# Kernel optimization log

Hardware: AMD Instinct MI355X
Metric: run time of the kernel (lower is better)

The kernel has to match this reference:

```python
import jax, jax.numpy as jnp
import numpy as np

W_MATCH, W_POS, W_COV = 1.0, 1.0, 0.1  # SetLoss init kwargs (w_rot unused in 3dpos path)


def setup_inputs() -> dict:
    key = jax.random.key(0)
    ks = jax.random.split(key, 6)
    bs, n, m = 4096, 31, 31
    B = bs * (n + 1)          # bs*(n+1) groups
    N = B * n                 # flattened rows
    # scores are 'in log space negative' -> use -softplus(randn)
    scores = -jax.nn.softplus(jax.random.normal(ks[0], (B, n + 1, m + 1), jnp.float32))
    indices = jax.random.randint(ks[1], (B, n, 1), -1, m)           # -1 = no prediction
    cov = jax.random.uniform(ks[2], (B, n, 1), jnp.float32, 0.1, 1.1)  # positive variances
    pos = jax.random.normal(ks[3], (B, n, 3), jnp.float32)
    pose = jax.random.normal(ks[4], (N, 7), jnp.float32)
    match = jax.random.randint(ks[5], (N, 1), -1, m)                # -1 = no label
    return {"scores": scores, "cov": cov, "pos": pos, "pose": pose,
            "indices": indices, "match": match}


def _masked_mean(vals, msk, default):
    cnt = msk.sum()
    s = jnp.where(msk, vals, 0.0).sum()
    return jnp.where(cnt > 0, s / jnp.maximum(cnt, 1).astype(vals.dtype), default)


def reference(scores, cov, pos, pose, indices, match):
    # SetLoss.forward(out, target, 'match_3dpos')
    m = scores.shape[2] - 1
    # ---- loss_match_func ----
    label_valid = match[:, 0] != -1                       # [N]
    li = jnp.where(match == -1, m, match)                 # route -1 to dustbin column m
    sc = scores[:, :-1, :].reshape(-1, m + 1)             # [N, m+1]
    cost = -jnp.take_along_axis(sc, li, axis=1)           # [N, 1]
    loss_match = cost.mean()
    oi = indices.reshape(-1, 1)
    success = (oi == match)[:, 0].astype(jnp.float32)     # [N]
    pred_valid = oi[:, 0] != -1
    recall = _masked_mean(success, label_valid, jnp.float32(1.0))
    precision = _masked_mean(success, pred_valid, jnp.float32(1.0))
    # ---- position MSE ----
    pos_f = pos.reshape(-1, 3)                            # [N, 3]
    d = pos_f - pose[:, :3]
    loss_pos = jnp.mean(d * d) * 3.0
    loss_rot = jnp.float32(0.0)
    # ---- diagonal-covariance NLL (loss_cov_func, dim=3, cov col repeated x3) ----
    # diag cov [c,c,c]: inverse = 1/c per entry, det = c**3
    c = cov.reshape(-1)                                   # [N]
    weighted = jnp.sum(d * d, axis=-1) / c                # diff^T Sigma^{-1} diff
    per = weighted + 3.0 * jnp.log(c) * 0.04              # + 0.04 * log det
    loss_cov = _masked_mean(per, pred_valid, jnp.float32(5.0))
    total = W_MATCH * loss_match + W_POS * loss_pos + W_COV * loss_cov
    return total, loss_match, loss_pos, loss_rot, loss_cov, precision, recall
```

## Files before the change

### kernel.cpp

```cpp
#include <hip/hip_runtime.h>
#include <hip/hip_bf16.h>

#define NRED 7

__device__ __forceinline__ float waveReduce(float v) {
#pragma unroll
    for (int o = 32; o > 0; o >>= 1) v += __shfl_down(v, o, 64);
    return v;
}

__global__ void setloss_partial(const float* __restrict__ scores,
                                const float* __restrict__ cov,
                                const float* __restrict__ pos,
                                const float* __restrict__ pose,
                                const int* __restrict__ indices,
                                const int* __restrict__ match,
                                float* __restrict__ part,
                                int N, int grid) {
    float acc[NRED];
#pragma unroll
    for (int k = 0; k < NRED; ++k) acc[k] = 0.0f;

    const int stride = gridDim.x * blockDim.x;
    for (int r = blockIdx.x * blockDim.x + threadIdx.x; r < N; r += stride) {
        const unsigned ur = (unsigned)r;
        const unsigned b  = ur / 31u;
        const unsigned i  = ur - b * 31u;

        const int mt = match[r];
        const int li = (mt < 0) ? 31 : mt;
        const float sc = scores[(size_t)(((b << 5) + i) << 5) + (unsigned)li];
        acc[0] -= sc;

        const int oi = indices[r];
        const float succ = (oi == mt) ? 1.0f : 0.0f;
        const bool lv = (mt != -1);
        const bool pv = (oi != -1);
        acc[1] += lv ? 1.0f : 0.0f;
        acc[2] += lv ? succ : 0.0f;
        acc[3] += pv ? 1.0f : 0.0f;
        acc[4] += pv ? succ : 0.0f;

        const float px = pos[3 * (size_t)r + 0];
        const float py = pos[3 * (size_t)r + 1];
        const float pz = pos[3 * (size_t)r + 2];
        const float qx = pose[7 * (size_t)r + 0];
        const float qy = pose[7 * (size_t)r + 1];
        const float qz = pose[7 * (size_t)r + 2];
        const float dx = px - qx, dy = py - qy, dz = pz - qz;
        const float d2 = dx * dx + dy * dy + dz * dz;
        acc[5] += d2;

        const float c = cov[r];
        if (pv) acc[6] += d2 / c + 0.12f * logf(c);
    }

    __shared__ float sdata[NRED][4];
    const int lane = threadIdx.x & 63;
    const int wave = threadIdx.x >> 6;
#pragma unroll
    for (int k = 0; k < NRED; ++k) {
        float v = waveReduce(acc[k]);
        if (lane == 0) sdata[k][wave] = v;
    }
    __syncthreads();
    if (threadIdx.x == 0) {
#pragma unroll
        for (int k = 0; k < NRED; ++k) {
            float v = sdata[k][0] + sdata[k][1] + sdata[k][2] + sdata[k][3];
            part[(size_t)k * grid + blockIdx.x] = v;
        }
    }
}

__global__ void setloss_final(const float* __restrict__ part, int grid,
                              float* __restrict__ out, int N) {
    float acc[NRED];
#pragma unroll
    for (int k = 0; k < NRED; ++k) acc[k] = 0.0f;
    for (int t = threadIdx.x; t < grid; t += blockDim.x) {
#pragma unroll
        for (int k = 0; k < NRED; ++k) acc[k] += part[(size_t)k * grid + t];
    }
    __shared__ float sdata[NRED][4];
    const int lane = threadIdx.x & 63;
    const int wave = threadIdx.x >> 6;
#pragma unroll
    for (int k = 0; k < NRED; ++k) {
        float v = waveReduce(acc[k]);
        if (lane == 0) sdata[k][wave] = v;
    }
    __syncthreads();
    if (threadIdx.x == 0) {
        float s[NRED];
#pragma unroll
        for (int k = 0; k < NRED; ++k)
            s[k] = sdata[k][0] + sdata[k][1] + sdata[k][2] + sdata[k][3];

        const float fN = (float)N;
        const float loss_match = s[0] / fN;
        const float loss_pos   = s[5] / fN;
        const float cnt_label  = s[1];
        const float cnt_pred   = s[3];
        const float recall     = (cnt_label > 0.0f) ? s[2] / cnt_label : 1.0f;
        const float precision  = (cnt_pred  > 0.0f) ? s[4] / cnt_pred  : 1.0f;
        const float loss_cov   = (cnt_pred  > 0.0f) ? s[6] / cnt_pred  : 5.0f;
        const float total = 1.0f * loss_match + 1.0f * loss_pos + 0.1f * loss_cov;

        out[0] = total;
        out[1] = loss_match;
        out[2] = loss_pos;
        out[3] = 0.0f;
        out[4] = loss_cov;
        out[5] = precision;
        out[6] = recall;
    }
}

extern "C" void kernel_launch(void* const* d_in, const int* in_sizes, int n_in,
                              void* d_out, int out_size, void* d_ws, size_t ws_size,
                              hipStream_t stream) {
    const float* scores  = (const float*)d_in[0];
    const float* cov     = (const float*)d_in[1];
    const float* pos     = (const float*)d_in[2];
    const float* pose    = (const float*)d_in[3];
    const int*   indices = (const int*)d_in[4];
    const int*   match   = (const int*)d_in[5];
    float* out = (float*)d_out;

    const int N = in_sizes[5];

    int grid = 2048;
    const size_t need = (size_t)NRED * (size_t)grid * sizeof(float);
    if (ws_size < need) grid = (int)(ws_size / ((size_t)NRED * sizeof(float)));
    if (grid < 1) grid = 1;

    float* part = (float*)d_ws;

    setloss_partial<<<grid, 256, 0, stream>>>(scores, cov, pos, pose, indices,
                                              match, part, N, grid);
    setloss_final<<<1, 256, 0, stream>>>(part, grid, out, N);
}
```

Baseline: 133.6 us.

## Vectorize row loads four-at-a-time and size grid to one chunk per thread

Each thread now processes four consecutive rows, loading match/indices/cov with int4/float4 and the pos and pose rows with several float4 loads, instead of strided scalar loads. The grid is sized so each thread handles about one chunk, giving far more blocks than the previous fixed 2048. This targets the poorly coalesced strided loads of the 3- and 7-wide rows. In exchange, the pose loads now pull all 7 columns, including the 4 unused ones, and the final reduction must sum many more partials.

```diff
diff --git a/kernel.cpp b/kernel.cpp
--- a/kernel.cpp
+++ b/kernel.cpp
@@ -9,50 +9,76 @@
     return v;
 }
 
-__global__ void setloss_partial(const float* __restrict__ scores,
-                                const float* __restrict__ cov,
-                                const float* __restrict__ pos,
-                                const float* __restrict__ pose,
-                                const int* __restrict__ indices,
-                                const int* __restrict__ match,
-                                float* __restrict__ part,
-                                int N, int grid) {
+__device__ __forceinline__ void rowAcc(int r, int mt, int oi, float c,
+                                       float px, float py, float pz,
+                                       float qx, float qy, float qz,
+                                       const float* __restrict__ scores,
+                                       float acc[NRED]) {
+    const unsigned ur = (unsigned)r;
+    const unsigned b  = ur / 31u;
+    const unsigned i  = ur - b * 31u;
+    const int li = (mt < 0) ? 31 : mt;
+    const float sc = scores[(size_t)b * 1024u + i * 32u + (unsigned)li];
+    acc[0] -= sc;
+
+    const float succ = (oi == mt) ? 1.0f : 0.0f;
+    const bool lv = (mt != -1);
+    const bool pv = (oi != -1);
+    acc[1] += lv ? 1.0f : 0.0f;
+    acc[2] += lv ? succ : 0.0f;
+    acc[3] += pv ? 1.0f : 0.0f;
+    acc[4] += pv ? succ : 0.0f;
+
+    const float dx = px - qx, dy = py - qy, dz = pz - qz;
+    const float d2 = dx * dx + dy * dy + dz * dz;
+    acc[5] += d2;
+    if (pv) acc[6] += d2 / c + 0.12f * logf(c);
+}
+
+__global__ __launch_bounds__(256) void setloss_partial(
+        const float* __restrict__ scores,
+        const float* __restrict__ cov,
+        const float* __restrict__ pos,
+        const float* __restrict__ pose,
+        const int* __restrict__ indices,
+        const int* __restrict__ match,
+        float* __restrict__ part,
+        int N, int grid, int nChunk) {
     float acc[NRED];
 #pragma unroll
     for (int k = 0; k < NRED; ++k) acc[k] = 0.0f;
 
-    const int stride = gridDim.x * blockDim.x;
-    for (int r = blockIdx.x * blockDim.x + threadIdx.x; r < N; r += stride) {
-        const unsigned ur = (unsigned)r;
-        const unsigned b  = ur / 31u;
-        const unsigned i  = ur - b * 31u;
+    const int tstride = grid * 256;
+    for (int chunk = blockIdx.x * 256 + threadIdx.x; chunk < nChunk; chunk += tstride) {
+        const int base = chunk * 4;
+        if (base + 3 < N) {
+            const int4   mm = *(const int4*)  (match   + base);
+            const int4   oo = *(const int4*)  (indices + base);
+            const float4 cc = *(const float4*)(cov     + base);
+            const float* pp = pos  + 3 * (size_t)base;
+            const float4 p0 = *(const float4*)(pp + 0);
+            const float4 p1 = *(const float4*)(pp + 4);
+            const float4 p2 = *(const float4*)(pp + 8);
+            const float* qq = pose + 7 * (size_t)base;
+            const float4 q0 = *(const float4*)(qq + 0);
+            const float4 q1 = *(const float4*)(qq + 4);
+            const float4 q2 = *(const float4*)(qq + 8);
+            const float4 q3 = *(const float4*)(qq + 12);
+            const float4 q4 = *(const float4*)(qq + 16);
+            const float4 q5 = *(const float4*)(qq + 20);
 
-        const int mt = match[r];
-        const int li = (mt < 0) ? 31 : mt;
-        const float sc = scores[(size_t)(((b << 5) + i) << 5) + (unsigned)li];
-        acc[0] -= sc;
-
-        const int oi = indices[r];
-        const float succ = (oi == mt) ? 1.0f : 0.0f;
-        const bool lv = (mt != -1);
-        const bool pv = (oi != -1);
-        acc[1] += lv ? 1.0f : 0.0f;
-        acc[2] += lv ? succ : 0.0f;
-        acc[3] += pv ? 1.0f : 0.0f;
-        acc[4] += pv ? succ : 0.0f;
-
-        const float px = pos[3 * (size_t)r + 0];
-        const float py = pos[3 * (size_t)r + 1];
-        const float pz = pos[3 * (size_t)r + 2];
-        const float qx = pose[7 * (size_t)r + 0];
-        const float qy = pose[7 * (size_t)r + 1];
-        const float qz = pose[7 * (size_t)r + 2];
-        const float dx = px - qx, dy = py - qy, dz = pz - qz;
-        const float d2 = dx * dx + dy * dy + dz * dz;
-        acc[5] += d2;
-
-        const float c = cov[r];
-        if (pv) acc[6] += d2 / c + 0.12f * logf(c);
+            rowAcc(base + 0, mm.x, oo.x, cc.x, p0.x, p0.y, p0.z, q0.x, q0.y, q0.z, scores, acc);
+            rowAcc(base + 1, mm.y, oo.y, cc.y, p0.w, p1.x, p1.y, q1.w, q2.x, q2.y, scores, acc);
+            rowAcc(base + 2, mm.z, oo.z, cc.z, p1.z, p1.w, p2.x, q3.z, q3.w, q4.x, scores, acc);
+            rowAcc(base + 3, mm.w, oo.w, cc.w, p2.y, p2.z, p2.w, q5.y, q5.z, q5.w, scores, acc);
+        } else {
+            for (int r = base; r < N; ++r) {
+                rowAcc(r, match[r], indices[r], cov[r],
+                       pos[3 * (size_t)r + 0], pos[3 * (size_t)r + 1], pos[3 * (size_t)r + 2],
+                       pose[7 * (size_t)r + 0], pose[7 * (size_t)r + 1], pose[7 * (size_t)r + 2],
+                       scores, acc);
+            }
+        }
     }
 
     __shared__ float sdata[NRED][4];
@@ -66,10 +92,8 @@
     __syncthreads();
     if (threadIdx.x == 0) {
 #pragma unroll
-        for (int k = 0; k < NRED; ++k) {
-            float v = sdata[k][0] + sdata[k][1] + sdata[k][2] + sdata[k][3];
-            part[(size_t)k * grid + blockIdx.x] = v;
-        }
+        for (int k = 0; k < NRED; ++k)
+            part[(size_t)k * grid + blockIdx.x] = sdata[k][0] + sdata[k][1] + sdata[k][2] + sdata[k][3];
     }
 }
 
@@ -105,7 +129,7 @@
         const float recall     = (cnt_label > 0.0f) ? s[2] / cnt_label : 1.0f;
         const float precision  = (cnt_pred  > 0.0f) ? s[4] / cnt_pred  : 1.0f;
         const float loss_cov   = (cnt_pred  > 0.0f) ? s[6] / cnt_pred  : 5.0f;
-        const float total = 1.0f * loss_match + 1.0f * loss_pos + 0.1f * loss_cov;
+        const float total = loss_match + loss_pos + 0.1f * loss_cov;
 
         out[0] = total;
         out[1] = loss_match;
@@ -129,15 +153,16 @@
     float* out = (float*)d_out;
 
     const int N = in_sizes[5];
+    const int nChunk = (N + 3) / 4;
 
-    int grid = 2048;
-    const size_t need = (size_t)NRED * (size_t)grid * sizeof(float);
-    if (ws_size < need) grid = (int)(ws_size / ((size_t)NRED * sizeof(float)));
+    int grid = (nChunk + 255) / 256;
+    const size_t cap = ws_size / ((size_t)NRED * sizeof(float));
+    if ((size_t)grid > cap) grid = (int)cap;
     if (grid < 1) grid = 1;
 
     float* part = (float*)d_ws;
 
     setloss_partial<<<grid, 256, 0, stream>>>(scores, cov, pos, pose, indices,
-                                              match, part, N, grid);
+                                              match, part, N, grid, nChunk);
     setloss_final<<<1, 256, 0, stream>>>(part, grid, out, N);
 }
```

New measurement: 136.1 us. About the same (+1.9%).
